# Optimization experiments

Hardware: AMD Instinct MI355X
Metric: run time of the kernel (lower is better)

Reference implementation:

```python
import jax, jax.numpy as jnp
import numpy as np
from jax import lax

B, FEA, C, DIM_OUT, HEADS, H, W = 4, 3, 256, 256, 8, 32, 32
EPS = 1e-5


def setup_inputs() -> dict:
    key = jax.random.key(0)
    ks = jax.random.split(key, 10)
    return {
        "x": jax.random.normal(ks[0], (B, C, H, W), jnp.float32),
        "query": jax.random.normal(ks[1], (B, FEA * H * W, C), jnp.float32),
        "conv_q_w": jax.random.normal(ks[2], (FEA, C, 1, 3, 3), jnp.float32) * 0.1,
        "bn_q_gamma": jnp.ones((FEA, C), jnp.float32),
        "bn_q_beta": jnp.zeros((FEA, C), jnp.float32),
        "bn_q_mean": jnp.zeros((FEA, C), jnp.float32),
        "bn_q_var": jnp.ones((FEA, C), jnp.float32),
        "conv_k_w": jax.random.normal(ks[3], (C, 1, 3, 3), jnp.float32) * 0.1,
        "bn_k_gamma": jnp.ones((C,), jnp.float32),
        "bn_k_beta": jnp.zeros((C,), jnp.float32),
        "bn_k_mean": jnp.zeros((C,), jnp.float32),
        "bn_k_var": jnp.ones((C,), jnp.float32),
        "conv_v_w": jax.random.normal(ks[4], (C, 1, 3, 3), jnp.float32) * 0.1,
        "bn_v_gamma": jnp.ones((C,), jnp.float32),
        "bn_v_beta": jnp.zeros((C,), jnp.float32),
        "bn_v_mean": jnp.zeros((C,), jnp.float32),
        "bn_v_var": jnp.ones((C,), jnp.float32),
        "proj_q_w": jax.random.normal(ks[5], (DIM_OUT, C), jnp.float32) * 0.02,
        "proj_k_w": jax.random.normal(ks[6], (DIM_OUT, C), jnp.float32) * 0.02,
        "proj_v_w": jax.random.normal(ks[7], (DIM_OUT, C), jnp.float32) * 0.02,
        "proj_w": jax.random.normal(ks[8], (DIM_OUT, DIM_OUT), jnp.float32) * 0.02,
        "proj_b": jnp.zeros((DIM_OUT,), jnp.float32),
        "h": H,
        "w": W,
    }


def _dw_conv_bn(x, w, gamma, beta, mean, var):
    # x: [B, C, H, W]; w: [C, 1, 3, 3] depthwise; BN in eval mode (running stats)
    y = lax.conv_general_dilated(
        x, w, window_strides=(1, 1), padding="SAME",
        feature_group_count=x.shape[1],
        dimension_numbers=("NCHW", "OIHW", "NCHW"))
    inv = gamma * lax.rsqrt(var + EPS)
    return y * inv[None, :, None, None] + (beta - mean * inv)[None, :, None, None]


def reference(x, query, conv_q_w, bn_q_gamma, bn_q_beta, bn_q_mean, bn_q_var,
              conv_k_w, bn_k_gamma, bn_k_beta, bn_k_mean, bn_k_var,
              conv_v_w, bn_v_gamma, bn_v_beta, bn_v_mean, bn_v_var,
              proj_q_w, proj_k_w, proj_v_w, proj_w, proj_b, h, w):
    b, c = x.shape[0], x.shape[1]
    res = h * w
    # split query into fea_no maps, depthwise conv + BN each, concat tokens
    q_parts = []
    for i in range(FEA):
        qi = query[:, res * i:res * (i + 1), :].reshape(b, h, w, c).transpose(0, 3, 1, 2)
        qi = _dw_conv_bn(qi, conv_q_w[i], bn_q_gamma[i], bn_q_beta[i], bn_q_mean[i], bn_q_var[i])
        q_parts.append(qi.reshape(b, c, res).transpose(0, 2, 1))  # [B, h*w, C]
    q_tok = jnp.concatenate(q_parts, axis=1)                      # [B, FEA*h*w, C]
    k_tok = _dw_conv_bn(x, conv_k_w, bn_k_gamma, bn_k_beta, bn_k_mean, bn_k_var)
    k_tok = k_tok.reshape(b, c, res).transpose(0, 2, 1)           # [B, h*w, C]
    v_tok = _dw_conv_bn(x, conv_v_w, bn_v_gamma, bn_v_beta, bn_v_mean, bn_v_var)
    v_tok = v_tok.reshape(b, c, res).transpose(0, 2, 1)
    hd = DIM_OUT // HEADS
    q = (q_tok @ proj_q_w.T).reshape(b, -1, HEADS, hd).transpose(0, 2, 1, 3)  # [B,H,L,d]
    k = (k_tok @ proj_k_w.T).reshape(b, -1, HEADS, hd).transpose(0, 2, 1, 3)  # [B,H,T,d]
    v = (v_tok @ proj_v_w.T).reshape(b, -1, HEADS, hd).transpose(0, 2, 1, 3)
    scale = DIM_OUT ** (-0.5)  # note: original scales by dim_out, not head_dim
    attn = jax.nn.softmax(jnp.einsum("bhld,bhtd->bhlt", q, k) * scale, axis=-1)
    out = jnp.einsum("bhlt,bhtd->bhld", attn, v)
    out = out.transpose(0, 2, 1, 3).reshape(b, -1, DIM_OUT)
    return out @ proj_w.T + proj_b
```

## Files before the change

kernel.cpp:

```cpp
#include <hip/hip_runtime.h>
#include <hip/hip_bf16.h>
#include <math.h>

#define B_     4
#define C_     256
#define RES_   1024
#define FEA_   3
#define LQ_    3072
#define HEADS_ 8
#define EPS_   1e-5f

typedef __bf16 bf16x8 __attribute__((ext_vector_type(8)));
typedef float  f32x16 __attribute__((ext_vector_type(16)));
typedef unsigned int uint4e __attribute__((ext_vector_type(4)));

#if __has_builtin(__builtin_amdgcn_exp2f)
#define EXP2(x) __builtin_amdgcn_exp2f(x)
#else
#define EXP2(x) exp2f(x)
#endif

__device__ __forceinline__ unsigned short bfbits(float v) {
    return __builtin_bit_cast(unsigned short, (__bf16)v);
}
__device__ __forceinline__ unsigned int pkbf(float lo, float hi2) {
    return (unsigned int)bfbits(lo) | ((unsigned int)bfbits(hi2) << 16);
}

__global__ __launch_bounds__(256) void pre_kernel(
    const float* __restrict__ query, const float* __restrict__ x,
    const float* __restrict__ wq,
    const float* __restrict__ gq, const float* __restrict__ bq,
    const float* __restrict__ mq, const float* __restrict__ vq,
    const float* __restrict__ wk, const float* __restrict__ gk, const float* __restrict__ bk,
    const float* __restrict__ mk, const float* __restrict__ vk,
    const float* __restrict__ wv, const float* __restrict__ gv, const float* __restrict__ bv,
    const float* __restrict__ mv, const float* __restrict__ vv,
    const float* __restrict__ pw0, const float* __restrict__ pw1,
    const float* __restrict__ pw2, const float* __restrict__ pw3,
    __bf16* __restrict__ q_tok, float* __restrict__ k_tok, float* __restrict__ v_tok,
    __bf16* __restrict__ Wq, __bf16* __restrict__ Wk,
    __bf16* __restrict__ Wv, __bf16* __restrict__ Wo)
{
    __shared__ float plane[RES_];
    int blk = blockIdx.x, tid = threadIdx.x;

    if (blk < 768) {
        int b = blk / 192, rem = blk % 192;
        int part = rem >> 6, t = rem & 63;
        int y0 = (t >> 3) * 4, x0 = (t & 7) * 4;
        int c = tid;
        const float* wp = wq + (size_t)(part * 256 + c) * 9;
        const float* qb = query + ((size_t)b * LQ_ + (size_t)part * 1024) * 256 + c;

        float w[9];
#pragma unroll
        for (int i = 0; i < 9; ++i) w[i] = wp[i];

        float v[6][6];
#pragma unroll
        for (int iy = 0; iy < 6; ++iy) {
            int yy = y0 - 1 + iy;
#pragma unroll
            for (int ix = 0; ix < 6; ++ix) {
                int xx = x0 - 1 + ix;
                bool ok = ((unsigned)yy < 32u) && ((unsigned)xx < 32u);
                v[iy][ix] = ok ? qb[(size_t)(yy * 32 + xx) * 256] : 0.f;
            }
        }
        int gi = part * 256 + c;
        float inv = gq[gi] * rsqrtf(vq[gi] + EPS_);
        float sh  = bq[gi] - mq[gi] * inv;
#pragma unroll
        for (int yi = 0; yi < 4; ++yi) {
#pragma unroll
            for (int xi = 0; xi < 4; ++xi) {
                float acc = 0.f;
#pragma unroll
                for (int ky = 0; ky < 3; ++ky)
#pragma unroll
                    for (int kj = 0; kj < 3; ++kj)
                        acc = fmaf(w[ky * 3 + kj], v[yi + ky][xi + kj], acc);
                int l = part * 1024 + (y0 + yi) * 32 + x0 + xi;
                q_tok[((size_t)b * LQ_ + l) * 256 + c] = (__bf16)fmaf(acc, inv, sh);
            }
        }
    } else if (blk < 2816) {
        int idx = blk - 768;
        int c = idx & 255, b = (idx >> 8) & 3, which = idx >> 10;
        const float* xp = x + ((size_t)b * 256 + c) * RES_;
#pragma unroll
        for (int i = 0; i < 4; ++i) plane[tid + i * 256] = xp[tid + i * 256];
        __syncthreads();

        const float* wp = (which ? wv : wk) + (size_t)c * 9;
        float w[9];
#pragma unroll
        for (int i = 0; i < 9; ++i) w[i] = wp[i];
        float inv = (which ? gv : gk)[c] * rsqrtf((which ? vv : vk)[c] + EPS_);
        float sh  = (which ? bv : bk)[c] - (which ? mv : mk)[c] * inv;
        float* out = (which ? v_tok : k_tok) + ((size_t)b * 256 + c) * RES_;
#pragma unroll
        for (int i0 = 0; i0 < 4; ++i0) {
            int p = tid + i0 * 256;
            int y = p >> 5, xx = p & 31;
            float acc = 0.f;
#pragma unroll
            for (int ky = 0; ky < 3; ++ky) {
                int yy = y + ky - 1;
                if ((unsigned)yy >= 32u) continue;
#pragma unroll
                for (int kx = 0; kx < 3; ++kx) {
                    int x2 = xx + kx - 1;
                    if ((unsigned)x2 >= 32u) continue;
                    acc = fmaf(w[ky * 3 + kx], plane[yy * 32 + x2], acc);
                }
            }
            out[p] = fmaf(acc, inv, sh);
        }
    } else {
        int idx = blk - 2816;
        int m = idx >> 6;
        const float* s = m == 0 ? pw0 : m == 1 ? pw1 : m == 2 ? pw2 : pw3;
        __bf16*      d = m == 0 ? Wq  : m == 1 ? Wk  : m == 2 ? Wv  : Wo;
        int i = ((idx & 63) * 256 + tid) * 4;
        float4 v = *(const float4*)(s + i);
        ushort4 u;
        u.x = bfbits(v.x); u.y = bfbits(v.y); u.z = bfbits(v.z); u.w = bfbits(v.w);
        *(ushort4*)(d + i) = u;
    }
}

__global__ __launch_bounds__(256) void gemm_kv_kernel(
    const float* __restrict__ kt, const float* __restrict__ vt,
    const __bf16* __restrict__ Wk, const __bf16* __restrict__ Wv,
    __bf16* __restrict__ Kb, __bf16* __restrict__ VT)
{
    int tid = threadIdx.x, lane = tid & 63, l31 = lane & 31, hi = lane >> 5;
    int gid = blockIdx.x * 4 + (tid >> 6);

    f32x16 acc;
#pragma unroll
    for (int r = 0; r < 16; ++r) acc[r] = 0.f;

    if (gid < 1024) {
        int g = gid;
        int b = g >> 8, rem = g & 255;
        int j0 = (rem >> 3) * 32, i0 = (rem & 7) * 32;
        const float* Bbase = kt + (size_t)b * 256 * RES_ + j0 + l31;
        const __bf16* Ap = Wk + (size_t)(i0 + l31) * 256 + 8 * hi;
#pragma unroll
        for (int k0 = 0; k0 < 256; k0 += 16) {
            bf16x8 bfr;
#pragma unroll
            for (int jj = 0; jj < 8; ++jj)
                bfr[jj] = (__bf16)Bbase[(size_t)(k0 + 8 * hi + jj) * RES_];
            acc = __builtin_amdgcn_mfma_f32_32x32x16_bf16(
                *(const bf16x8*)(Ap + k0), bfr, acc, 0, 0, 0);
        }
        int head = i0 >> 5;
        __bf16* op = Kb + ((size_t)(b * HEADS_ + head) * RES_ + j0 + l31) * 32 + 4 * hi;
#pragma unroll
        for (int rr = 0; rr < 4; ++rr) {
            ushort4 u;
            u.x = bfbits(acc[4 * rr + 0]); u.y = bfbits(acc[4 * rr + 1]);
            u.z = bfbits(acc[4 * rr + 2]); u.w = bfbits(acc[4 * rr + 3]);
            *(ushort4*)(op + 8 * rr) = u;
        }
    } else {
        int g = gid - 1024;
        int b = g >> 8, rem = g & 255;
        int i0t = (rem >> 3) * 32, j0 = (rem & 7) * 32;
        const float* Abase = vt + (size_t)b * 256 * RES_ + i0t + l31;
        const __bf16* Bp = Wv + (size_t)(j0 + l31) * 256 + 8 * hi;
#pragma unroll
        for (int k0 = 0; k0 < 256; k0 += 16) {
            bf16x8 afr;
#pragma unroll
            for (int jj = 0; jj < 8; ++jj)
                afr[jj] = (__bf16)Abase[(size_t)(k0 + 8 * hi + jj) * RES_];
            acc = __builtin_amdgcn_mfma_f32_32x32x16_bf16(
                afr, *(const bf16x8*)(Bp + k0), acc, 0, 0, 0);
        }
        int head = j0 >> 5;
        __bf16* op = VT + ((size_t)(b * HEADS_ + head) * 32 + l31) * RES_ + i0t + 4 * hi;
#pragma unroll
        for (int rr = 0; rr < 4; ++rr) {
            ushort4 u;
            u.x = bfbits(acc[4 * rr + 0]); u.y = bfbits(acc[4 * rr + 1]);
            u.z = bfbits(acc[4 * rr + 2]); u.w = bfbits(acc[4 * rr + 3]);
            *(ushort4*)(op + 8 * rr) = u;
        }
    }
}

__global__ __launch_bounds__(256) void gemm_out_kernel(
    const __bf16* __restrict__ Oc, const __bf16* __restrict__ Wo,
    const float* __restrict__ bias, float* __restrict__ out)
{
    int tid = threadIdx.x, lane = tid & 63, l31 = lane & 31, hi = lane >> 5;
    int gid = blockIdx.x * 4 + (tid >> 6);
    int b = gid / 768, rem = gid % 768;
    int j0 = (rem >> 3) * 32, i0 = (rem & 7) * 32;
    const __bf16* Bp = Oc + ((size_t)b * LQ_ + j0 + l31) * 256 + 8 * hi;
    const __bf16* Ap = Wo + (size_t)(i0 + l31) * 256 + 8 * hi;

    f32x16 acc;
#pragma unroll
    for (int r = 0; r < 16; ++r) acc[r] = 0.f;
#pragma unroll
    for (int k0 = 0; k0 < 256; k0 += 16) {
        acc = __builtin_amdgcn_mfma_f32_32x32x16_bf16(
            *(const bf16x8*)(Ap + k0), *(const bf16x8*)(Bp + k0), acc, 0, 0, 0);
    }
    float* op = out + ((size_t)b * LQ_ + j0 + l31) * 256 + i0 + 4 * hi;
#pragma unroll
    for (int rr = 0; rr < 4; ++rr) {
        float4 bv = *(const float4*)(bias + i0 + 4 * hi + 8 * rr);
        float4 r4;
        r4.x = acc[4 * rr + 0] + bv.x; r4.y = acc[4 * rr + 1] + bv.y;
        r4.z = acc[4 * rr + 2] + bv.z; r4.w = acc[4 * rr + 3] + bv.w;
        *(float4*)(op + 8 * rr) = r4;
    }
}

__global__ __launch_bounds__(256, 4) void attn_mfma_kernel(
    const __bf16* __restrict__ qt, const __bf16* __restrict__ Wq,
    const __bf16* __restrict__ Kb, const __bf16* __restrict__ VT,
    __bf16* __restrict__ Oc)
{
    __shared__ float Os[3][64][35];
    __shared__ __bf16 Qlds[64][40];

    int tid  = threadIdx.x;
    int lane = tid & 63, l31 = lane & 31, hi = lane >> 5;
    int th   = tid >> 6;

    int i    = blockIdx.x;
    int xcd  = i & 7, slot = i >> 3;
    int bh   = xcd * 4 + slot / 48;
    int q0   = (slot % 48) * 64;
    int b    = bh >> 3, h = bh & 7;

    if (th < 2) {
        const __bf16* Bp = qt + ((size_t)b * LQ_ + q0 + th * 32 + l31) * 256 + 8 * hi;
        const __bf16* Ap = Wq + (size_t)(h * 32 + l31) * 256 + 8 * hi;
        f32x16 acc;
#pragma unroll
        for (int r = 0; r < 16; ++r) acc[r] = 0.f;
#pragma unroll
        for (int k0 = 0; k0 < 256; k0 += 16) {
            acc = __builtin_amdgcn_mfma_f32_32x32x16_bf16(
                *(const bf16x8*)(Ap + k0), *(const bf16x8*)(Bp + k0), acc, 0, 0, 0);
        }
        const float scale = 0.0625f * 1.44269504f;
        __bf16* qp = &Qlds[th * 32 + l31][4 * hi];
#pragma unroll
        for (int rr = 0; rr < 4; ++rr) {
            ushort4 u;
            u.x = bfbits(acc[4 * rr + 0] * scale); u.y = bfbits(acc[4 * rr + 1] * scale);
            u.z = bfbits(acc[4 * rr + 2] * scale); u.w = bfbits(acc[4 * rr + 3] * scale);
            *(ushort4*)(qp + 8 * rr) = u;
        }
    }
    __syncthreads();

    const __bf16* qbase = &Qlds[l31][8 * hi];
    bf16x8 qA0 = *(const bf16x8*)qbase;
    bf16x8 qA1 = *(const bf16x8*)(qbase + 16);
    bf16x8 qB0 = *(const bf16x8*)(qbase + 32 * 40);
    bf16x8 qB1 = *(const bf16x8*)(qbase + 32 * 40 + 16);

    const __bf16* kp = Kb + ((size_t)bh * RES_ + th * 256 + l31) * 32 + 8 * hi;
    const __bf16* vp = VT + ((size_t)bh * 32 + l31) * RES_ + th * 256 + 8 * hi;

    f32x16 oA, oB;
#pragma unroll
    for (int r = 0; r < 16; ++r) { oA[r] = 0.f; oB[r] = 0.f; }
    float lsA = 0.f, lsB = 0.f;

    auto smpack = [&](const f32x16& s, float& ls, bf16x8& pb1, bf16x8& pb2) {
        float p[16];
#pragma unroll
        for (int r = 0; r < 16; ++r) p[r] = EXP2(s[r]);
        float t0 = (p[0]+p[1]) + (p[2]+p[3]);
        float t1 = (p[4]+p[5]) + (p[6]+p[7]);
        float t2 = (p[8]+p[9]) + (p[10]+p[11]);
        float t3 = (p[12]+p[13]) + (p[14]+p[15]);
        ls += (t0 + t1) + (t2 + t3);

        unsigned int w0 = pkbf(p[0],  p[1]),  w1 = pkbf(p[2],  p[3]);
        unsigned int w2 = pkbf(p[4],  p[5]),  w3 = pkbf(p[6],  p[7]);
        unsigned int w4 = pkbf(p[8],  p[9]),  w5 = pkbf(p[10], p[11]);
        unsigned int w6 = pkbf(p[12], p[13]), w7 = pkbf(p[14], p[15]);

        asm("v_permlane32_swap_b32 %0, %1" : "+v"(w0), "+v"(w2));
        asm("v_permlane32_swap_b32 %0, %1" : "+v"(w1), "+v"(w3));
        asm("v_permlane32_swap_b32 %0, %1" : "+v"(w4), "+v"(w6));
        asm("v_permlane32_swap_b32 %0, %1" : "+v"(w5), "+v"(w7));

        uint4e b1 = { w0, w1, w2, w3 };
        uint4e b2 = { w4, w5, w6, w7 };
        pb1 = __builtin_bit_cast(bf16x8, b1);
        pb2 = __builtin_bit_cast(bf16x8, b2);
    };

    bf16x8 kc0 = *(const bf16x8*)kp;
    bf16x8 kc1 = *(const bf16x8*)(kp + 16);

#pragma unroll
    for (int st = 0; st < 8; ++st) {
        const __bf16* vc = vp + (size_t)st * 32;
        bf16x8 V0 = *(const bf16x8*)vc;
        bf16x8 V1 = *(const bf16x8*)(vc + 16);

        bf16x8 kn0, kn1;
        if (st < 7) {
            const __bf16* kn = kp + (size_t)(st + 1) * 1024;
            kn0 = *(const bf16x8*)kn;
            kn1 = *(const bf16x8*)(kn + 16);
        }

        f32x16 sA, sB;
#pragma unroll
        for (int r = 0; r < 16; ++r) { sA[r] = 0.f; sB[r] = 0.f; }
        __builtin_amdgcn_s_setprio(1);
        sA = __builtin_amdgcn_mfma_f32_32x32x16_bf16(kc0, qA0, sA, 0, 0, 0);
        sB = __builtin_amdgcn_mfma_f32_32x32x16_bf16(kc0, qB0, sB, 0, 0, 0);
        sA = __builtin_amdgcn_mfma_f32_32x32x16_bf16(kc1, qA1, sA, 0, 0, 0);
        sB = __builtin_amdgcn_mfma_f32_32x32x16_bf16(kc1, qB1, sB, 0, 0, 0);
        __builtin_amdgcn_s_setprio(0);

        bf16x8 pA1, pA2, pB1, pB2;
        smpack(sA, lsA, pA1, pA2);
        smpack(sB, lsB, pB1, pB2);

        __builtin_amdgcn_s_setprio(1);
        oA = __builtin_amdgcn_mfma_f32_32x32x16_bf16(V0, pA1, oA, 0, 0, 0);
        oB = __builtin_amdgcn_mfma_f32_32x32x16_bf16(V0, pB1, oB, 0, 0, 0);
        oA = __builtin_amdgcn_mfma_f32_32x32x16_bf16(V1, pA2, oA, 0, 0, 0);
        oB = __builtin_amdgcn_mfma_f32_32x32x16_bf16(V1, pB2, oB, 0, 0, 0);
        __builtin_amdgcn_s_setprio(0);

        if (st < 7) { kc0 = kn0; kc1 = kn1; }
    }

    lsA += __shfl_xor(lsA, 32, 64);
    lsB += __shfl_xor(lsB, 32, 64);

    __syncthreads();
    if (th) {
#pragma unroll
        for (int r = 0; r < 16; ++r) {
            Os[th - 1][lane][r]      = oA[r];
            Os[th - 1][lane][17 + r] = oB[r];
        }
        Os[th - 1][lane][16] = lsA;
        Os[th - 1][lane][33] = lsB;
    }
    __syncthreads();
    if (!th) {
        float lA = lsA + Os[0][lane][16] + Os[1][lane][16] + Os[2][lane][16];
        float lB = lsB + Os[0][lane][33] + Os[1][lane][33] + Os[2][lane][33];
        float invA = 1.0f / lA, invB = 1.0f / lB;
        __bf16* opA = Oc + ((size_t)b * LQ_ + q0 + l31) * 256 + h * 32 + 4 * hi;
        __bf16* opB = opA + (size_t)32 * 256;
#pragma unroll
        for (int rr = 0; rr < 4; ++rr) {
            ushort4 ua, ub;
            ua.x = bfbits((oA[4*rr+0] + Os[0][lane][4*rr+0] + Os[1][lane][4*rr+0] + Os[2][lane][4*rr+0]) * invA);
            ua.y = bfbits((oA[4*rr+1] + Os[0][lane][4*rr+1] + Os[1][lane][4*rr+1] + Os[2][lane][4*rr+1]) * invA);
            ua.z = bfbits((oA[4*rr+2] + Os[0][lane][4*rr+2] + Os[1][lane][4*rr+2] + Os[2][lane][4*rr+2]) * invA);
            ua.w = bfbits((oA[4*rr+3] + Os[0][lane][4*rr+3] + Os[1][lane][4*rr+3] + Os[2][lane][4*rr+3]) * invA);
            ub.x = bfbits((oB[4*rr+0] + Os[0][lane][17+4*rr+0] + Os[1][lane][17+4*rr+0] + Os[2][lane][17+4*rr+0]) * invB);
            ub.y = bfbits((oB[4*rr+1] + Os[0][lane][17+4*rr+1] + Os[1][lane][17+4*rr+1] + Os[2][lane][17+4*rr+1]) * invB);
            ub.z = bfbits((oB[4*rr+2] + Os[0][lane][17+4*rr+2] + Os[1][lane][17+4*rr+2] + Os[2][lane][17+4*rr+2]) * invB);
            ub.w = bfbits((oB[4*rr+3] + Os[0][lane][17+4*rr+3] + Os[1][lane][17+4*rr+3] + Os[2][lane][17+4*rr+3]) * invB);
            *(ushort4*)(opA + 8 * rr) = ua;
            *(ushort4*)(opB + 8 * rr) = ub;
        }
    }
}

extern "C" void kernel_launch(void* const* d_in, const int* in_sizes, int n_in,
                              void* d_out, int out_size, void* d_ws, size_t ws_size,
                              hipStream_t stream) {
    const float* x        = (const float*)d_in[0];
    const float* query    = (const float*)d_in[1];
    const float* conv_q_w = (const float*)d_in[2];
    const float* bn_q_g   = (const float*)d_in[3];
    const float* bn_q_b   = (const float*)d_in[4];
    const float* bn_q_m   = (const float*)d_in[5];
    const float* bn_q_v   = (const float*)d_in[6];
    const float* conv_k_w = (const float*)d_in[7];
    const float* bn_k_g   = (const float*)d_in[8];
    const float* bn_k_b   = (const float*)d_in[9];
    const float* bn_k_m   = (const float*)d_in[10];
    const float* bn_k_v   = (const float*)d_in[11];
    const float* conv_v_w = (const float*)d_in[12];
    const float* bn_v_g   = (const float*)d_in[13];
    const float* bn_v_b   = (const float*)d_in[14];
    const float* bn_v_m   = (const float*)d_in[15];
    const float* bn_v_v   = (const float*)d_in[16];
    const float* proj_q_w = (const float*)d_in[17];
    const float* proj_k_w = (const float*)d_in[18];
    const float* proj_v_w = (const float*)d_in[19];
    const float* proj_w   = (const float*)d_in[20];
    const float* proj_b   = (const float*)d_in[21];

    char* ws = (char*)d_ws;
    __bf16* q_tok = (__bf16*)(ws + 0);
    float*  k_tok = (float*) (ws + 6291456);
    float*  v_tok = (float*) (ws + 10485760);
    __bf16* Kb    = (__bf16*)(ws + 14680064);
    __bf16* VT    = (__bf16*)(ws + 16777216);
    __bf16* Wq    = (__bf16*)(ws + 18874368);
    __bf16* Wk    = (__bf16*)(ws + 19005440);
    __bf16* Wv    = (__bf16*)(ws + 19136512);
    __bf16* Wo    = (__bf16*)(ws + 19267584);
    __bf16* Oc    = (__bf16*)(ws + 19398656);
    float*  out   = (float*)d_out;

    pre_kernel<<<dim3(3072), 256, 0, stream>>>(
        query, x, conv_q_w, bn_q_g, bn_q_b, bn_q_m, bn_q_v,
        conv_k_w, bn_k_g, bn_k_b, bn_k_m, bn_k_v,
        conv_v_w, bn_v_g, bn_v_b, bn_v_m, bn_v_v,
        proj_q_w, proj_k_w, proj_v_w, proj_w,
        q_tok, k_tok, v_tok, Wq, Wk, Wv, Wo);

    gemm_kv_kernel<<<dim3(512), 256, 0, stream>>>(
        k_tok, v_tok, Wk, Wv, Kb, VT);

    attn_mfma_kernel<<<dim3(1536), 256, 0, stream>>>(q_tok, Wq, Kb, VT, Oc);

    gemm_out_kernel<<<dim3(768), 256, 0, stream>>>(Oc, Wo, proj_b, out);
}
```

Measured before the change: 71.78 us.

## Fuse K/V depthwise convs per plane, store K/V tokens as bf16

The K and V depthwise conv+BN blocks are merged so each block loads one x plane into shared memory and produces both K and V outputs. This halves the x reads and the block count of the pre kernel. The conv outputs are written as bf16 instead of fp32, which halves the intermediate traffic into gemm_kv_kernel and removes its conversion step. The workspace layout shrinks to match. The attention kernel also moves the bf16 packing and permlane swaps ahead of the row-sum reduction, and drops a __syncthreads before the Os epilogue. That last removal is a risk if Os shares shared memory with earlier data still in use.

Result: no change. 70.61 us (-1.6%).

```diff
diff --git a/kernel.cpp b/kernel.cpp
--- a/kernel.cpp
+++ b/kernel.cpp
@@ -38,7 +38,7 @@
     const float* __restrict__ mv, const float* __restrict__ vv,
     const float* __restrict__ pw0, const float* __restrict__ pw1,
     const float* __restrict__ pw2, const float* __restrict__ pw3,
-    __bf16* __restrict__ q_tok, float* __restrict__ k_tok, float* __restrict__ v_tok,
+    __bf16* __restrict__ q_tok, __bf16* __restrict__ k_tok, __bf16* __restrict__ v_tok,
     __bf16* __restrict__ Wq, __bf16* __restrict__ Wk,
     __bf16* __restrict__ Wv, __bf16* __restrict__ Wo)
 {
@@ -85,26 +85,30 @@
                 q_tok[((size_t)b * LQ_ + l) * 256 + c] = (__bf16)fmaf(acc, inv, sh);
             }
         }
-    } else if (blk < 2816) {
+    } else if (blk < 1792) {
         int idx = blk - 768;
-        int c = idx & 255, b = (idx >> 8) & 3, which = idx >> 10;
+        int c = idx & 255, b = idx >> 8;
         const float* xp = x + ((size_t)b * 256 + c) * RES_;
 #pragma unroll
         for (int i = 0; i < 4; ++i) plane[tid + i * 256] = xp[tid + i * 256];
         __syncthreads();
 
-        const float* wp = (which ? wv : wk) + (size_t)c * 9;
-        float w[9];
-#pragma unroll
-        for (int i = 0; i < 9; ++i) w[i] = wp[i];
-        float inv = (which ? gv : gk)[c] * rsqrtf((which ? vv : vk)[c] + EPS_);
-        float sh  = (which ? bv : bk)[c] - (which ? mv : mk)[c] * inv;
-        float* out = (which ? v_tok : k_tok) + ((size_t)b * 256 + c) * RES_;
+        const float* wpk = wk + (size_t)c * 9;
+        const float* wpv = wv + (size_t)c * 9;
+        float wkr[9], wvr[9];
+#pragma unroll
+        for (int i = 0; i < 9; ++i) { wkr[i] = wpk[i]; wvr[i] = wpv[i]; }
+        float invK = gk[c] * rsqrtf(vk[c] + EPS_);
+        float shK  = bk[c] - mk[c] * invK;
+        float invV = gv[c] * rsqrtf(vv[c] + EPS_);
+        float shV  = bv[c] - mv[c] * invV;
+        __bf16* outK = k_tok + ((size_t)b * 256 + c) * RES_;
+        __bf16* outV = v_tok + ((size_t)b * 256 + c) * RES_;
 #pragma unroll
         for (int i0 = 0; i0 < 4; ++i0) {
             int p = tid + i0 * 256;
             int y = p >> 5, xx = p & 31;
-            float acc = 0.f;
+            float aK = 0.f, aV = 0.f;
 #pragma unroll
             for (int ky = 0; ky < 3; ++ky) {
                 int yy = y + ky - 1;
@@ -113,13 +117,16 @@
                 for (int kx = 0; kx < 3; ++kx) {
                     int x2 = xx + kx - 1;
                     if ((unsigned)x2 >= 32u) continue;
-                    acc = fmaf(w[ky * 3 + kx], plane[yy * 32 + x2], acc);
+                    float pv = plane[yy * 32 + x2];
+                    aK = fmaf(wkr[ky * 3 + kx], pv, aK);
+                    aV = fmaf(wvr[ky * 3 + kx], pv, aV);
                 }
             }
-            out[p] = fmaf(acc, inv, sh);
+            outK[p] = (__bf16)fmaf(aK, invK, shK);
+            outV[p] = (__bf16)fmaf(aV, invV, shV);
         }
     } else {
-        int idx = blk - 2816;
+        int idx = blk - 1792;
         int m = idx >> 6;
         const float* s = m == 0 ? pw0 : m == 1 ? pw1 : m == 2 ? pw2 : pw3;
         __bf16*      d = m == 0 ? Wq  : m == 1 ? Wk  : m == 2 ? Wv  : Wo;
@@ -132,7 +139,7 @@
 }
 
 __global__ __launch_bounds__(256) void gemm_kv_kernel(
-    const float* __restrict__ kt, const float* __restrict__ vt,
+    const __bf16* __restrict__ kt, const __bf16* __restrict__ vt,
     const __bf16* __restrict__ Wk, const __bf16* __restrict__ Wv,
     __bf16* __restrict__ Kb, __bf16* __restrict__ VT)
 {
@@ -147,14 +154,14 @@
         int g = gid;
         int b = g >> 8, rem = g & 255;
         int j0 = (rem >> 3) * 32, i0 = (rem & 7) * 32;
-        const float* Bbase = kt + (size_t)b * 256 * RES_ + j0 + l31;
+        const __bf16* Bbase = kt + (size_t)b * 256 * RES_ + j0 + l31;
         const __bf16* Ap = Wk + (size_t)(i0 + l31) * 256 + 8 * hi;
 #pragma unroll
         for (int k0 = 0; k0 < 256; k0 += 16) {
             bf16x8 bfr;
 #pragma unroll
             for (int jj = 0; jj < 8; ++jj)
-                bfr[jj] = (__bf16)Bbase[(size_t)(k0 + 8 * hi + jj) * RES_];
+                bfr[jj] = Bbase[(size_t)(k0 + 8 * hi + jj) * RES_];
             acc = __builtin_amdgcn_mfma_f32_32x32x16_bf16(
                 *(const bf16x8*)(Ap + k0), bfr, acc, 0, 0, 0);
         }
@@ -171,14 +178,14 @@
         int g = gid - 1024;
         int b = g >> 8, rem = g & 255;
         int i0t = (rem >> 3) * 32, j0 = (rem & 7) * 32;
-        const float* Abase = vt + (size_t)b * 256 * RES_ + i0t + l31;
+        const __bf16* Abase = vt + (size_t)b * 256 * RES_ + i0t + l31;
         const __bf16* Bp = Wv + (size_t)(j0 + l31) * 256 + 8 * hi;
 #pragma unroll
         for (int k0 = 0; k0 < 256; k0 += 16) {
             bf16x8 afr;
 #pragma unroll
             for (int jj = 0; jj < 8; ++jj)
-                afr[jj] = (__bf16)Abase[(size_t)(k0 + 8 * hi + jj) * RES_];
+                afr[jj] = Abase[(size_t)(k0 + 8 * hi + jj) * RES_];
             acc = __builtin_amdgcn_mfma_f32_32x32x16_bf16(
                 afr, *(const bf16x8*)(Bp + k0), acc, 0, 0, 0);
         }
@@ -283,26 +290,27 @@
         float p[16];
 #pragma unroll
         for (int r = 0; r < 16; ++r) p[r] = EXP2(s[r]);
+
+        unsigned int w0 = pkbf(p[0],  p[1]),  w1 = pkbf(p[2],  p[3]);
+        unsigned int w2 = pkbf(p[4],  p[5]),  w3 = pkbf(p[6],  p[7]);
+        unsigned int w4 = pkbf(p[8],  p[9]),  w5 = pkbf(p[10], p[11]);
+        unsigned int w6 = pkbf(p[12], p[13]), w7 = pkbf(p[14], p[15]);
+
+        asm("v_permlane32_swap_b32 %0, %1" : "+v"(w0), "+v"(w2));
+        asm("v_permlane32_swap_b32 %0, %1" : "+v"(w1), "+v"(w3));
+        asm("v_permlane32_swap_b32 %0, %1" : "+v"(w4), "+v"(w6));
+        asm("v_permlane32_swap_b32 %0, %1" : "+v"(w5), "+v"(w7));
+
+        uint4e b1 = { w0, w1, w2, w3 };
+        uint4e b2 = { w4, w5, w6, w7 };
+        pb1 = __builtin_bit_cast(bf16x8, b1);
+        pb2 = __builtin_bit_cast(bf16x8, b2);
+
         float t0 = (p[0]+p[1]) + (p[2]+p[3]);
         float t1 = (p[4]+p[5]) + (p[6]+p[7]);
         float t2 = (p[8]+p[9]) + (p[10]+p[11]);
         float t3 = (p[12]+p[13]) + (p[14]+p[15]);
         ls += (t0 + t1) + (t2 + t3);
-
-        unsigned int w0 = pkbf(p[0],  p[1]),  w1 = pkbf(p[2],  p[3]);
-        unsigned int w2 = pkbf(p[4],  p[5]),  w3 = pkbf(p[6],  p[7]);
-        unsigned int w4 = pkbf(p[8],  p[9]),  w5 = pkbf(p[10], p[11]);
-        unsigned int w6 = pkbf(p[12], p[13]), w7 = pkbf(p[14], p[15]);
-
-        asm("v_permlane32_swap_b32 %0, %1" : "+v"(w0), "+v"(w2));
-        asm("v_permlane32_swap_b32 %0, %1" : "+v"(w1), "+v"(w3));
-        asm("v_permlane32_swap_b32 %0, %1" : "+v"(w4), "+v"(w6));
-        asm("v_permlane32_swap_b32 %0, %1" : "+v"(w5), "+v"(w7));
-
-        uint4e b1 = { w0, w1, w2, w3 };
-        uint4e b2 = { w4, w5, w6, w7 };
-        pb1 = __builtin_bit_cast(bf16x8, b1);
-        pb2 = __builtin_bit_cast(bf16x8, b2);
     };
 
     bf16x8 kc0 = *(const bf16x8*)kp;
@@ -348,7 +356,6 @@
     lsA += __shfl_xor(lsA, 32, 64);
     lsB += __shfl_xor(lsB, 32, 64);
 
-    __syncthreads();
     if (th) {
 #pragma unroll
         for (int r = 0; r < 16; ++r) {
@@ -410,18 +417,18 @@
 
     char* ws = (char*)d_ws;
     __bf16* q_tok = (__bf16*)(ws + 0);
-    float*  k_tok = (float*) (ws + 6291456);
-    float*  v_tok = (float*) (ws + 10485760);
-    __bf16* Kb    = (__bf16*)(ws + 14680064);
-    __bf16* VT    = (__bf16*)(ws + 16777216);
-    __bf16* Wq    = (__bf16*)(ws + 18874368);
-    __bf16* Wk    = (__bf16*)(ws + 19005440);
-    __bf16* Wv    = (__bf16*)(ws + 19136512);
-    __bf16* Wo    = (__bf16*)(ws + 19267584);
-    __bf16* Oc    = (__bf16*)(ws + 19398656);
+    __bf16* k_tok = (__bf16*)(ws + 6291456);
+    __bf16* v_tok = (__bf16*)(ws + 8388608);
+    __bf16* Kb    = (__bf16*)(ws + 10485760);
+    __bf16* VT    = (__bf16*)(ws + 12582912);
+    __bf16* Wq    = (__bf16*)(ws + 14680064);
+    __bf16* Wk    = (__bf16*)(ws + 14811136);
+    __bf16* Wv    = (__bf16*)(ws + 14942208);
+    __bf16* Wo    = (__bf16*)(ws + 15073280);
+    __bf16* Oc    = (__bf16*)(ws + 15204352);
     float*  out   = (float*)d_out;
 
-    pre_kernel<<<dim3(3072), 256, 0, stream>>>(
+    pre_kernel<<<dim3(2048), 256, 0, stream>>>(
         query, x, conv_q_w, bn_q_g, bn_q_b, bn_q_m, bn_q_v,
         conv_k_w, bn_k_g, bn_k_b, bn_k_m, bn_k_v,
         conv_v_w, bn_v_g, bn_v_b, bn_v_m, bn_v_v,
```
